# Optimization experiments

Measured on AMD Instinct MI355X. Metric: run time of the kernel, lower is better.

## Reference

```python
import jax, jax.numpy as jnp
import numpy as np

SEQ_LEN, IN_CH, OUT_CH, H, BATCH = 2048, 16, 1, 80, 512


def _lstm(x, W_ih, W_hh, b_ih, b_hh):
    """Single-layer batch-first LSTM (PyTorch gate order i,f,g,o).
    x: [B, T, D]. Returns (outputs [B, T, H], last hidden [B, H])."""
    B = x.shape[0]
    h0 = jnp.zeros((B, H), x.dtype)
    c0 = jnp.zeros((B, H), x.dtype)
    # Precompute input projections for all timesteps in one GEMM: [T, B, 4H]
    xproj = jnp.einsum('btd,gd->tbg', x, W_ih) + (b_ih + b_hh)

    def step(carry, xp_t):
        h, c = carry
        gates = xp_t + h @ W_hh.T  # [B, 4H]
        i, f, g, o = jnp.split(gates, 4, axis=-1)
        i = jax.nn.sigmoid(i)
        f = jax.nn.sigmoid(f)
        g = jnp.tanh(g)
        o = jax.nn.sigmoid(o)
        c = f * c + i * g
        h = o * jnp.tanh(c)
        return (h, c), h

    (h_last, _), hs = jax.lax.scan(step, (h0, c0), xproj)
    return jnp.swapaxes(hs, 0, 1), h_last


def setup_inputs() -> dict:
    key = jax.random.key(0)
    ks = jax.random.split(key, 12)
    s1 = 1.0 / np.sqrt(H)
    d = {
        'x': jax.random.normal(ks[0], (BATCH, SEQ_LEN, IN_CH), jnp.float32),
        'W_ih1': jax.random.uniform(ks[1], (4 * H, IN_CH), jnp.float32, -s1, s1),
        'W_hh1': jax.random.uniform(ks[2], (4 * H, H), jnp.float32, -s1, s1),
        'b_ih1': jax.random.uniform(ks[3], (4 * H,), jnp.float32, -s1, s1),
        'b_hh1': jax.random.uniform(ks[4], (4 * H,), jnp.float32, -s1, s1),
        'W_ih2': jax.random.uniform(ks[5], (4 * H, H), jnp.float32, -s1, s1),
        'W_hh2': jax.random.uniform(ks[6], (4 * H, H), jnp.float32, -s1, s1),
        'b_ih2': jax.random.uniform(ks[7], (4 * H,), jnp.float32, -s1, s1),
        'b_hh2': jax.random.uniform(ks[8], (4 * H,), jnp.float32, -s1, s1),
        'W_d': jax.random.uniform(ks[9], (OUT_CH, H), jnp.float32, -s1, s1),
        'b_d': jax.random.uniform(ks[10], (OUT_CH,), jnp.float32, -s1, s1),
    }
    return d


def reference(x, W_ih1, W_hh1, b_ih1, b_hh1, W_ih2, W_hh2, b_ih2, b_hh2, W_d, b_d):
    B = x.shape[0]
    x = x.reshape((B, SEQ_LEN, IN_CH))
    y1, _ = _lstm(x, W_ih1, W_hh1, b_ih1, b_hh1)          # [B, T, H]
    _, h_last = _lstm(y1, W_ih2, W_hh2, b_ih2, b_hh2)     # [B, H]
    return h_last @ W_d.T + b_d                           # [B, OUT_CH]
```

## Files before the change

### kernel.cpp

```cpp
#include <hip/hip_runtime.h>

#define T_SEQ 2048
#define DIN   16
#define HH    80
#define NTHR  512
#define NBLK  256
#define BT    2
#define ROWE  160
#define XRT   512
#define XCH   128

#define L2E   1.44269504088896340736f

typedef _Float16 f16x8 __attribute__((ext_vector_type(8)));
typedef float    f32x4 __attribute__((ext_vector_type(4)));

__device__ __forceinline__ float rcp_fast(float x){ return __builtin_amdgcn_rcpf(x); }
__device__ __forceinline__ float ex2(float x){
#if __has_builtin(__builtin_amdgcn_exp2f)
    return __builtin_amdgcn_exp2f(x);
#else
    return exp2f(x);
#endif
}

#define MF(av, bv, cv) __builtin_amdgcn_mfma_f32_16x16x32_f16(av, bv, cv, 0, 0, 0)
#define L1SLOT(acc, s) { acc = MF(A[s][0], B0, Q[s]); acc = MF(A[s][1], B1, acc); \
                         acc = MF(A[s][2], B2, acc); }
#define L2SLOT(acc, s) { acc = MF(A[s][0], B0, Q[s]); acc = MF(A[s][1], B1, acc); \
                         acc = MF(A[s][2], B2, acc); acc = MF(A[s][3], B3, acc); \
                         acc = MF(A[s][4], B4, acc); }

__global__
__attribute__((amdgpu_flat_work_group_size(NTHR, NTHR)))
__attribute__((amdgpu_waves_per_eu(2, 2)))
void lstm2_mfma(
    const float* __restrict__ x,
    const float* __restrict__ W_ih1, const float* __restrict__ W_hh1,
    const float* __restrict__ b_ih1, const float* __restrict__ b_hh1,
    const float* __restrict__ W_ih2, const float* __restrict__ W_hh2,
    const float* __restrict__ b_ih2, const float* __restrict__ b_hh2,
    const float* __restrict__ W_d,   const float* __restrict__ b_d,
    float* __restrict__ out)
{
    __shared__ __align__(16) _Float16 HB[2][BT][ROWE];
    __shared__ __align__(16) _Float16 XR[XRT][BT][DIN];

    const int t    = threadIdx.x;
    const int lane = t & 63;
    const int wv   = t >> 6;
    const bool isL1w = (wv < 4);
    const int m16  = lane & 15;
    const int kgrp = lane >> 4;
    const int b0   = blockIdx.x * BT;

    const int uloc = isL1w ? 20*wv : 20*(wv-4);

    f16x8 A[5][5];
    f32x4 Q[5];
    {
        const int g  = m16 & 3;
        const int ut = m16 >> 2;
        const float sc = (g == 2) ? (2.f*L2E) : L2E;
        #pragma unroll
        for (int s = 0; s < 5; ++s) {
            const int grow = g*HH + (uloc + 4*s + ut);
            #pragma unroll
            for (int c = 0; c < 5; ++c) {
                if (isL1w && c >= 3) continue;
                f16x8 a;
                #pragma unroll
                for (int j = 0; j < 8; ++j) {
                    const int kk = 32*c + 8*kgrp + j;
                    const float v = isL1w
                        ? ((kk < DIN) ? W_ih1[(size_t)grow*DIN + kk]
                                      : W_hh1[(size_t)grow*HH + (kk - DIN)])
                        : ((kk < HH)  ? W_ih2[(size_t)grow*HH + kk]
                                      : W_hh2[(size_t)grow*HH + (kk - HH)]);
                    a[j] = (_Float16)(v * sc);
                }
                A[s][c] = a;
            }
            const int u = uloc + 4*s + kgrp;
            const float* bI = isL1w ? b_ih1 : b_ih2;
            const float* bH = isL1w ? b_hh1 : b_hh2;
            f32x4 bb;
            bb[0] = (bI[       u] + bH[       u]) * L2E;
            bb[1] = (bI[  HH + u] + bH[  HH + u]) * L2E;
            bb[2] = (bI[2*HH + u] + bH[2*HH + u]) * (2.f*L2E);
            bb[3] = (bI[3*HH + u] + bH[3*HH + u]) * L2E;
            Q[s] = bb;
        }
    }

    const int  te      = m16 >> 1;
    const bool act_ep  = (m16 < 10);
    const int  unit_ep = uloc + 4*(act_ep ? te : 0) + kgrp;
    const int  seg     = isL1w ? 0 : HH;
    const int  batch_ep = lane & 1;

    for (int i = t; i < 2*BT*ROWE; i += NTHR) ((_Float16*)HB)[i] = (_Float16)0.f;

    const int toff = t >> 2, xb = (t >> 1) & 1, c8 = t & 1;
    const float* xsrc = x + ((size_t)(b0 + xb) * T_SEQ) * DIN + c8*8;
    #pragma unroll
    for (int c0 = 0; c0 < 2*XCH; c0 += XCH) {
        const int tt = c0 + toff;
        const float4 va = *(const float4*)(xsrc + (size_t)tt * DIN);
        const float4 vb = *(const float4*)(xsrc + (size_t)tt * DIN + 4);
        f16x8 h;
        h[0]=(_Float16)va.x; h[1]=(_Float16)va.y; h[2]=(_Float16)va.z; h[3]=(_Float16)va.w;
        h[4]=(_Float16)vb.x; h[5]=(_Float16)vb.y; h[6]=(_Float16)vb.z; h[7]=(_Float16)vb.w;
        *(f16x8*)&XR[tt][xb][c8*8] = h;
    }
    __syncthreads();

    float cst = 0.f;
    float4 xva{}, xvb{};
    int pend_tt = -1;

    #pragma unroll 1
    for (int k = 0; k <= T_SEQ; ++k) {
        const int pb = k & 1, nb = pb ^ 1;

        if ((k & (XCH-1)) == 0 && (k + 2*XCH + XCH) <= T_SEQ + XCH) {
            const int tt = k + 2*XCH + toff;
            if (tt < T_SEQ) {
                xva = *(const float4*)(xsrc + (size_t)tt * DIN);
                xvb = *(const float4*)(xsrc + (size_t)tt * DIN + 4);
                pend_tt = tt;
            }
        } else if ((k & (XCH-1)) == 1 && pend_tt >= 0) {
            f16x8 h;
            h[0]=(_Float16)xva.x; h[1]=(_Float16)xva.y; h[2]=(_Float16)xva.z; h[3]=(_Float16)xva.w;
            h[4]=(_Float16)xvb.x; h[5]=(_Float16)xvb.y; h[6]=(_Float16)xvb.z; h[7]=(_Float16)xvb.w;
            *(f16x8*)&XR[pend_tt & (XRT-1)][xb][c8*8] = h;
            pend_tt = -1;
        }

        const bool act = isL1w ? (k < T_SEQ) : (k >= 1);
        if (act) {
            const _Float16* hb = &HB[pb][lane & 1][0];
            f32x4 acc0, acc1, acc2, acc3, acc4;
            if (isL1w) {
                const _Float16* xrb = &XR[k & (XRT-1)][lane & 1][0];
                const _Float16* p0  = (kgrp < 2) ? (xrb + 8*kgrp) : (hb + 8*kgrp - 16);
                const f16x8 B0 = *(const f16x8*)p0;
                const f16x8 B1 = *(const f16x8*)(hb + 16 + 8*kgrp);
                const f16x8 B2 = *(const f16x8*)(hb + 48 + 8*kgrp);
                L1SLOT(acc0, 0) L1SLOT(acc1, 1) L1SLOT(acc2, 2)
                L1SLOT(acc3, 3) L1SLOT(acc4, 4)
            } else {
                const f16x8 B0 = *(const f16x8*)(hb +       8*kgrp);
                const f16x8 B1 = *(const f16x8*)(hb +  32 + 8*kgrp);
                const f16x8 B2 = *(const f16x8*)(hb +  64 + 8*kgrp);
                const f16x8 B3 = *(const f16x8*)(hb +  96 + 8*kgrp);
                const f16x8 B4 = *(const f16x8*)(hb + 128 + 8*kgrp);
                L2SLOT(acc0, 0) L2SLOT(acc1, 1) L2SLOT(acc2, 2)
                L2SLOT(acc3, 3) L2SLOT(acc4, 4)
            }

            float M0 = acc0[0], M1 = acc0[1], M2 = acc0[2], M3 = acc0[3];
            if (te == 1) { M0 = acc1[0]; M1 = acc1[1]; M2 = acc1[2]; M3 = acc1[3]; }
            if (te == 2) { M0 = acc2[0]; M1 = acc2[1]; M2 = acc2[2]; M3 = acc2[3]; }
            if (te == 3) { M0 = acc3[0]; M1 = acc3[1]; M2 = acc3[2]; M3 = acc3[3]; }
            if (te == 4) { M0 = acc4[0]; M1 = acc4[1]; M2 = acc4[2]; M3 = acc4[3]; }

            const float iv = rcp_fast(1.f + ex2(-M0));
            const float fv = rcp_fast(1.f + ex2(-M1));
            const float gv = 1.f - 2.f*rcp_fast(1.f + ex2(M2));
            const float ov = rcp_fast(1.f + ex2(-M3));
            cst = fv*cst + iv*gv;
            const float tc = 1.f - 2.f*rcp_fast(1.f + ex2(cst * (2.f*L2E)));
            if (act_ep)
                HB[nb][batch_ep][seg + unit_ep] = (_Float16)(ov * tc);
        }
        __syncthreads();
    }

    if (wv == 0) {
        float a0 = 0.f, a1 = 0.f;
        for (int u = lane; u < HH; u += 64) {
            const float wd = W_d[u];
            a0 += wd * (float)HB[1][0][HH + u];
            a1 += wd * (float)HB[1][1][HH + u];
        }
        #pragma unroll
        for (int off = 32; off > 0; off >>= 1) {
            a0 += __shfl_down(a0, off);
            a1 += __shfl_down(a1, off);
        }
        if (lane == 0) { out[b0] = a0 + b_d[0]; out[b0 + 1] = a1 + b_d[0]; }
    }
}

extern "C" void kernel_launch(void* const* d_in, const int* in_sizes, int n_in,
                              void* d_out, int out_size, void* d_ws, size_t ws_size,
                              hipStream_t stream) {
    const float* x     = (const float*)d_in[0];
    const float* W_ih1 = (const float*)d_in[1];
    const float* W_hh1 = (const float*)d_in[2];
    const float* b_ih1 = (const float*)d_in[3];
    const float* b_hh1 = (const float*)d_in[4];
    const float* W_ih2 = (const float*)d_in[5];
    const float* W_hh2 = (const float*)d_in[6];
    const float* b_ih2 = (const float*)d_in[7];
    const float* b_hh2 = (const float*)d_in[8];
    const float* W_d   = (const float*)d_in[9];
    const float* b_d   = (const float*)d_in[10];

    lstm2_mfma<<<NBLK, NTHR, 0, stream>>>(x, W_ih1, W_hh1, b_ih1, b_hh1,
                                          W_ih2, W_hh2, b_ih2, b_hh2,
                                          W_d, b_d, (float*)d_out);
}
```

Measured before the change: 1.459 ms.

## Replace per-step block barrier with LDS flag counters between layer wave groups

```diff
diff --git a/kernel.cpp b/kernel.cpp
--- a/kernel.cpp
+++ b/kernel.cpp
@@ -6,9 +6,7 @@
 #define NTHR  512
 #define NBLK  256
 #define BT    2
-#define ROWE  160
-#define XRT   512
-#define XCH   128
+#define ROWE  192
 
 #define L2E   1.44269504088896340736f
 
@@ -31,10 +29,19 @@
                          acc = MF(A[s][2], B2, acc); acc = MF(A[s][3], B3, acc); \
                          acc = MF(A[s][4], B4, acc); }
 
+#define SPIN2(pa, ta, pb, tb) { int _s = 0; \
+    while ((__hip_atomic_load((pa), __ATOMIC_RELAXED, __HIP_MEMORY_SCOPE_WORKGROUP) < (ta)) || \
+           (__hip_atomic_load((pb), __ATOMIC_RELAXED, __HIP_MEMORY_SCOPE_WORKGROUP) < (tb))) { \
+        if (++_s > (1<<14)) break; } \
+    __builtin_amdgcn_fence(__ATOMIC_ACQUIRE, "workgroup"); }
+
+#define SIGNAL(p) if (lane == 0) \
+    __hip_atomic_fetch_add((p), 1, __ATOMIC_RELEASE, __HIP_MEMORY_SCOPE_WORKGROUP)
+
 __global__
 __attribute__((amdgpu_flat_work_group_size(NTHR, NTHR)))
 __attribute__((amdgpu_waves_per_eu(2, 2)))
-void lstm2_mfma(
+void lstm2_flag(
     const float* __restrict__ x,
     const float* __restrict__ W_ih1, const float* __restrict__ W_hh1,
     const float* __restrict__ b_ih1, const float* __restrict__ b_hh1,
@@ -44,7 +51,9 @@
     float* __restrict__ out)
 {
     __shared__ __align__(16) _Float16 HB[2][BT][ROWE];
-    __shared__ __align__(16) _Float16 XR[XRT][BT][DIN];
+    __shared__ int W1c;
+    __shared__ int W2c;
+    __shared__ int RD2c;
 
     const int t    = threadIdx.x;
     const int lane = t & 63;
@@ -96,94 +105,113 @@
     const int  te      = m16 >> 1;
     const bool act_ep  = (m16 < 10);
     const int  unit_ep = uloc + 4*(act_ep ? te : 0) + kgrp;
-    const int  seg     = isL1w ? 0 : HH;
+    const int  seg     = isL1w ? DIN : (DIN + HH);
     const int  batch_ep = lane & 1;
 
     for (int i = t; i < 2*BT*ROWE; i += NTHR) ((_Float16*)HB)[i] = (_Float16)0.f;
-
-    const int toff = t >> 2, xb = (t >> 1) & 1, c8 = t & 1;
-    const float* xsrc = x + ((size_t)(b0 + xb) * T_SEQ) * DIN + c8*8;
-    #pragma unroll
-    for (int c0 = 0; c0 < 2*XCH; c0 += XCH) {
-        const int tt = c0 + toff;
-        const float4 va = *(const float4*)(xsrc + (size_t)tt * DIN);
-        const float4 vb = *(const float4*)(xsrc + (size_t)tt * DIN + 4);
-        f16x8 h;
-        h[0]=(_Float16)va.x; h[1]=(_Float16)va.y; h[2]=(_Float16)va.z; h[3]=(_Float16)va.w;
-        h[4]=(_Float16)vb.x; h[5]=(_Float16)vb.y; h[6]=(_Float16)vb.z; h[7]=(_Float16)vb.w;
-        *(f16x8*)&XR[tt][xb][c8*8] = h;
+    if (t == 0) { W1c = 0; W2c = 0; RD2c = 0; }
+
+    const int xbn = (lane >> 4) & 1;
+    const int xch = lane & 15;
+    const float* xptr = x + ((size_t)(b0 + xbn) * T_SEQ) * DIN + xch;
+    float xa = 0.f, xbv = 0.f, xcv = 0.f;
+    if (wv == 0 && lane < 32) {
+        HB[0][xbn][xch] = (_Float16)xptr[0];
+        xa  = xptr[1*DIN];
+        xbv = xptr[2*DIN];
+        xcv = xptr[3*DIN];
     }
     __syncthreads();
 
     float cst = 0.f;
-    float4 xva{}, xvb{};
-    int pend_tt = -1;
 
     #pragma unroll 1
     for (int k = 0; k <= T_SEQ; ++k) {
         const int pb = k & 1, nb = pb ^ 1;
 
-        if ((k & (XCH-1)) == 0 && (k + 2*XCH + XCH) <= T_SEQ + XCH) {
-            const int tt = k + 2*XCH + toff;
-            if (tt < T_SEQ) {
-                xva = *(const float4*)(xsrc + (size_t)tt * DIN);
-                xvb = *(const float4*)(xsrc + (size_t)tt * DIN + 4);
-                pend_tt = tt;
-            }
-        } else if ((k & (XCH-1)) == 1 && pend_tt >= 0) {
-            f16x8 h;
-            h[0]=(_Float16)xva.x; h[1]=(_Float16)xva.y; h[2]=(_Float16)xva.z; h[3]=(_Float16)xva.w;
-            h[4]=(_Float16)xvb.x; h[5]=(_Float16)xvb.y; h[6]=(_Float16)xvb.z; h[7]=(_Float16)xvb.w;
-            *(f16x8*)&XR[pend_tt & (XRT-1)][xb][c8*8] = h;
-            pend_tt = -1;
-        }
-
-        const bool act = isL1w ? (k < T_SEQ) : (k >= 1);
-        if (act) {
-            const _Float16* hb = &HB[pb][lane & 1][0];
-            f32x4 acc0, acc1, acc2, acc3, acc4;
-            if (isL1w) {
-                const _Float16* xrb = &XR[k & (XRT-1)][lane & 1][0];
-                const _Float16* p0  = (kgrp < 2) ? (xrb + 8*kgrp) : (hb + 8*kgrp - 16);
-                const f16x8 B0 = *(const f16x8*)p0;
-                const f16x8 B1 = *(const f16x8*)(hb + 16 + 8*kgrp);
-                const f16x8 B2 = *(const f16x8*)(hb + 48 + 8*kgrp);
+        if (isL1w) {
+            SPIN2(&W1c, 4*k, &RD2c, 4*k);
+
+            if (wv == 0 && lane < 32) {
+                HB[nb][xbn][xch] = (_Float16)xa;
+                xa = xbv; xbv = xcv;
+                const int tn = (k + 4 < T_SEQ) ? (k + 4) : (T_SEQ - 1);
+                xcv = xptr[(size_t)tn * DIN];
+            }
+
+            if (k < T_SEQ) {
+                const _Float16* rb = &HB[pb][lane & 1][0];
+                const f16x8 B0 = *(const f16x8*)(rb +       8*kgrp);
+                const f16x8 B1 = *(const f16x8*)(rb +  32 + 8*kgrp);
+                const f16x8 B2 = *(const f16x8*)(rb +  64 + 8*kgrp);
+                f32x4 acc0, acc1, acc2, acc3, acc4;
                 L1SLOT(acc0, 0) L1SLOT(acc1, 1) L1SLOT(acc2, 2)
                 L1SLOT(acc3, 3) L1SLOT(acc4, 4)
-            } else {
-                const f16x8 B0 = *(const f16x8*)(hb +       8*kgrp);
-                const f16x8 B1 = *(const f16x8*)(hb +  32 + 8*kgrp);
-                const f16x8 B2 = *(const f16x8*)(hb +  64 + 8*kgrp);
-                const f16x8 B3 = *(const f16x8*)(hb +  96 + 8*kgrp);
-                const f16x8 B4 = *(const f16x8*)(hb + 128 + 8*kgrp);
+
+                float M0 = acc0[0], M1 = acc0[1], M2 = acc0[2], M3 = acc0[3];
+                if (te == 1) { M0 = acc1[0]; M1 = acc1[1]; M2 = acc1[2]; M3 = acc1[3]; }
+                if (te == 2) { M0 = acc2[0]; M1 = acc2[1]; M2 = acc2[2]; M3 = acc2[3]; }
+                if (te == 3) { M0 = acc3[0]; M1 = acc3[1]; M2 = acc3[2]; M3 = acc3[3]; }
+                if (te == 4) { M0 = acc4[0]; M1 = acc4[1]; M2 = acc4[2]; M3 = acc4[3]; }
+
+                const float iv = rcp_fast(1.f + ex2(-M0));
+                const float fv = rcp_fast(1.f + ex2(-M1));
+                const float gv = 1.f - 2.f*rcp_fast(1.f + ex2(M2));
+                const float ov = rcp_fast(1.f + ex2(-M3));
+                cst = fv*cst + iv*gv;
+                const float tc = 1.f - 2.f*rcp_fast(1.f + ex2(cst * (2.f*L2E)));
+                if (act_ep)
+                    HB[nb][batch_ep][seg + unit_ep] = (_Float16)(ov * tc);
+            }
+            asm volatile("s_waitcnt lgkmcnt(0)" ::: "memory");
+            SIGNAL(&W1c);
+        } else {
+            SPIN2(&W1c, 4*k, &W2c, 4*k);
+
+            f16x8 B0{}, B1{}, B2{}, B3{}, B4{};
+            if (k >= 1) {
+                const _Float16* rb = &HB[pb][lane & 1][0];
+                B0 = *(const f16x8*)(rb +  16 + 8*kgrp);
+                B1 = *(const f16x8*)(rb +  48 + 8*kgrp);
+                B2 = *(const f16x8*)(rb +  80 + 8*kgrp);
+                B3 = *(const f16x8*)(rb + 112 + 8*kgrp);
+                B4 = *(const f16x8*)(rb + 144 + 8*kgrp);
+            }
+            asm volatile("s_waitcnt lgkmcnt(0)" ::: "memory");
+            SIGNAL(&RD2c);
+
+            if (k >= 1) {
+                f32x4 acc0, acc1, acc2, acc3, acc4;
                 L2SLOT(acc0, 0) L2SLOT(acc1, 1) L2SLOT(acc2, 2)
                 L2SLOT(acc3, 3) L2SLOT(acc4, 4)
-            }
-
-            float M0 = acc0[0], M1 = acc0[1], M2 = acc0[2], M3 = acc0[3];
-            if (te == 1) { M0 = acc1[0]; M1 = acc1[1]; M2 = acc1[2]; M3 = acc1[3]; }
-            if (te == 2) { M0 = acc2[0]; M1 = acc2[1]; M2 = acc2[2]; M3 = acc2[3]; }
-            if (te == 3) { M0 = acc3[0]; M1 = acc3[1]; M2 = acc3[2]; M3 = acc3[3]; }
-            if (te == 4) { M0 = acc4[0]; M1 = acc4[1]; M2 = acc4[2]; M3 = acc4[3]; }
-
-            const float iv = rcp_fast(1.f + ex2(-M0));
-            const float fv = rcp_fast(1.f + ex2(-M1));
-            const float gv = 1.f - 2.f*rcp_fast(1.f + ex2(M2));
-            const float ov = rcp_fast(1.f + ex2(-M3));
-            cst = fv*cst + iv*gv;
-            const float tc = 1.f - 2.f*rcp_fast(1.f + ex2(cst * (2.f*L2E)));
-            if (act_ep)
-                HB[nb][batch_ep][seg + unit_ep] = (_Float16)(ov * tc);
-        }
-        __syncthreads();
+
+                float M0 = acc0[0], M1 = acc0[1], M2 = acc0[2], M3 = acc0[3];
+                if (te == 1) { M0 = acc1[0]; M1 = acc1[1]; M2 = acc1[2]; M3 = acc1[3]; }
+                if (te == 2) { M0 = acc2[0]; M1 = acc2[1]; M2 = acc2[2]; M3 = acc2[3]; }
+                if (te == 3) { M0 = acc3[0]; M1 = acc3[1]; M2 = acc3[2]; M3 = acc3[3]; }
+                if (te == 4) { M0 = acc4[0]; M1 = acc4[1]; M2 = acc4[2]; M3 = acc4[3]; }
+
+                const float iv = rcp_fast(1.f + ex2(-M0));
+                const float fv = rcp_fast(1.f + ex2(-M1));
+                const float gv = 1.f - 2.f*rcp_fast(1.f + ex2(M2));
+                const float ov = rcp_fast(1.f + ex2(-M3));
+                cst = fv*cst + iv*gv;
+                const float tc = 1.f - 2.f*rcp_fast(1.f + ex2(cst * (2.f*L2E)));
+                if (act_ep)
+                    HB[nb][batch_ep][seg + unit_ep] = (_Float16)(ov * tc);
+            }
+            asm volatile("s_waitcnt lgkmcnt(0)" ::: "memory");
+            SIGNAL(&W2c);
+        }
     }
 
     if (wv == 0) {
+        SPIN2(&W2c, 4*(T_SEQ+1), &W1c, 0);
         float a0 = 0.f, a1 = 0.f;
         for (int u = lane; u < HH; u += 64) {
             const float wd = W_d[u];
-            a0 += wd * (float)HB[1][0][HH + u];
-            a1 += wd * (float)HB[1][1][HH + u];
+            a0 += wd * (float)HB[1][0][DIN + HH + u];
+            a1 += wd * (float)HB[1][1][DIN + HH + u];
         }
         #pragma unroll
         for (int off = 32; off > 0; off >>= 1) {
@@ -209,7 +237,7 @@
     const float* W_d   = (const float*)d_in[9];
     const float* b_d   = (const float*)d_in[10];
 
-    lstm2_mfma<<<NBLK, NTHR, 0, stream>>>(x, W_ih1, W_hh1, b_ih1, b_hh1,
+    lstm2_flag<<<NBLK, NTHR, 0, stream>>>(x, W_ih1, W_hh1, b_ih1, b_hh1,
                                           W_ih2, W_hh2, b_ih2, b_hh2,
                                           W_d, b_d, (float*)d_out);
 }
```

Measured after the change: 1.584 ms. 8.5% more time.
